# Kernel tuning notes

Measured on AMD Instinct MI355X. Metric: run time of the kernel, lower is better.

Reference implementation:

```python
import jax, jax.numpy as jnp
import numpy as np

D_MODEL = 1024
NUM_HEADS = 16
D_K = D_MODEL // NUM_HEADS
EPS = 1e-8  # torch F.cosine_similarity eps


def setup_inputs() -> dict:
    key = jax.random.key(0)
    ks = jax.random.split(key, 12)
    B, S = 2, 2048
    s = 1.0 / np.sqrt(D_MODEL)
    inp = {
        'q': jax.random.normal(ks[0], (B, S, D_MODEL), jnp.float32),
        'k': jax.random.normal(ks[1], (B, S, D_MODEL), jnp.float32),
        'v': jax.random.normal(ks[2], (B, S, D_MODEL), jnp.float32),
        'mask': jnp.ones((1, 1, 1, S), jnp.int32),
        'Wq': jax.random.normal(ks[3], (D_MODEL, D_MODEL), jnp.float32) * s,
        'bq': jax.random.normal(ks[4], (D_MODEL,), jnp.float32) * s,
        'Wk': jax.random.normal(ks[5], (D_MODEL, D_MODEL), jnp.float32) * s,
        'bk': jax.random.normal(ks[6], (D_MODEL,), jnp.float32) * s,
        'Wv': jax.random.normal(ks[7], (D_MODEL, D_MODEL), jnp.float32) * s,
        'bv': jax.random.normal(ks[8], (D_MODEL,), jnp.float32) * s,
        'Wo': jax.random.normal(ks[9], (D_MODEL, D_MODEL), jnp.float32) * s,
        'bo': jax.random.normal(ks[10], (D_MODEL,), jnp.float32) * s,
    }
    return inp


def _cosine(a, b):
    # torch F.cosine_similarity along last dim with eps clamp on each norm
    na = jnp.maximum(jnp.linalg.norm(a, axis=-1), EPS)
    nb = jnp.maximum(jnp.linalg.norm(b, axis=-1), EPS)
    return jnp.sum(a * b, axis=-1) / (na * nb)


def reference(q, k, v, mask, Wq, bq, Wk, bk, Wv, bv, Wo, bo):
    B, S, _ = q.shape
    H, dk = NUM_HEADS, D_K
    # projections -> [B, H, S, dk]
    def proj(x, W, b):
        return (x @ W.T + b).reshape(B, S, H, dk).transpose(0, 2, 1, 3)
    Q = proj(q, Wq, bq)
    K = proj(k, Wk, bk)
    V = proj(v, Wv, bv)
    scores = jnp.einsum('bhqd,bhkd->bhqk', Q, K) / np.sqrt(dk)
    # per-(batch, head) cosine-similarity bias between mean query and mean value
    cos = _cosine(Q.mean(axis=2), V.mean(axis=2))  # [B, H]
    bias = cos[:, :, None, None]
    scores = scores + bias * 0.5 + bias * 0.3  # empathy + equilibrium biases
    scores = jnp.where(mask == 0, -1e9, scores)
    probs = jax.nn.softmax(scores, axis=-1)
    attn = jnp.einsum('bhqk,bhkd->bhqd', probs, V)
    attn = attn.transpose(0, 2, 1, 3).reshape(B, S, H * dk)
    out = attn @ Wo.T + bo
    return out, jnp.mean(bias)
```

## Files before the change

### kernel.cpp

```cpp
#include <hip/hip_runtime.h>
#include <math.h>

#define SB 2
#define SS 2048
#define SD 1024
#define SH 16
#define SDK 64
#define MROWS (SB*SS)

#define L2E 1.44269504088896341f
#define SCL2E (0.125f * L2E)
#define M0 8.0f

typedef float  f32x4  __attribute__((ext_vector_type(4)));
typedef float  f32x16 __attribute__((ext_vector_type(16)));
typedef __bf16 bf16x8 __attribute__((ext_vector_type(8)));
typedef short  short8 __attribute__((ext_vector_type(8), may_alias));
typedef short  short4a __attribute__((ext_vector_type(4), may_alias));
typedef float  floatx4a __attribute__((ext_vector_type(4), may_alias));
typedef unsigned uint4v __attribute__((ext_vector_type(4)));

__device__ __forceinline__ short f2bf(float f) {
    unsigned u = __float_as_uint(f);
    u += 0x7fffu + ((u >> 16) & 1u);
    return (short)(u >> 16);
}
__device__ __forceinline__ float bf2f(short v) {
    return __uint_as_float(((unsigned)(unsigned short)v) << 16);
}
__device__ __forceinline__ bf16x8 ldb(const short* p) {
    short8 v = *(const short8*)p;
    return __builtin_bit_cast(bf16x8, v);
}
__device__ __forceinline__ unsigned cvtpk(float lo, float hi) {
    unsigned r;
    asm("v_cvt_pk_bf16_f32 %0, %1, %2" : "=v"(r) : "v"(lo), "v"(hi));
    return r;
}
__device__ __forceinline__ void gload16(const short* g, short* l) {
    __builtin_amdgcn_global_load_lds(
        (const __attribute__((address_space(1))) unsigned*)g,
        (__attribute__((address_space(3))) unsigned*)l, 16, 0, 0);
}
#define MFMA(a, b, c)   __builtin_amdgcn_mfma_f32_16x16x32_bf16((a), (b), (c), 0, 0, 0)
#define MFMA32(a, b, c) __builtin_amdgcn_mfma_f32_32x32x16_bf16((a), (b), (c), 0, 0, 0)

__global__ __launch_bounds__(256) void conv_all(
    const float* __restrict__ q, const float* __restrict__ k, const float* __restrict__ v,
    const float* __restrict__ Wq, const float* __restrict__ Wk,
    const float* __restrict__ Wv, const float* __restrict__ Wo,
    short* __restrict__ qb, short* __restrict__ kb, short* __restrict__ vb,
    short* __restrict__ wqb, short* __restrict__ wkb,
    short* __restrict__ wvb, short* __restrict__ wob)
{
    const int y = blockIdx.y;
    const float* src; short* dst; int n;
    switch (y) {
        case 0: src = q;  dst = qb;  n = MROWS * SD; break;
        case 1: src = k;  dst = kb;  n = MROWS * SD; break;
        case 2: src = v;  dst = vb;  n = MROWS * SD; break;
        case 3: src = Wq; dst = wqb; n = SD * SD; break;
        case 4: src = Wk; dst = wkb; n = SD * SD; break;
        case 5: src = Wv; dst = wvb; n = SD * SD; break;
        default: src = Wo; dst = wob; n = SD * SD; break;
    }
    int i = (blockIdx.x * 256 + threadIdx.x) * 4;
    if (i >= n) return;
    floatx4a x = *(const floatx4a*)(src + i);
    short4a o;
    o[0] = f2bf(x[0]); o[1] = f2bf(x[1]); o[2] = f2bf(x[2]); o[3] = f2bf(x[3]);
    *(short4a*)(dst + i) = o;
}

__global__ __launch_bounds__(256) void gemm128(
    const short* __restrict__ X0, const short* __restrict__ X1, const short* __restrict__ X2,
    const short* __restrict__ W0, const short* __restrict__ W1, const short* __restrict__ W2,
    const float* __restrict__ bias0, const float* __restrict__ bias1, const float* __restrict__ bias2,
    short* __restrict__ O0, short* __restrict__ O1, short* __restrict__ O2)
{
    const int z = blockIdx.z;
    const short* X = (z == 0) ? X0 : (z == 1) ? X1 : X2;
    const short* W = (z == 0) ? W0 : (z == 1) ? W1 : W2;
    const float* Bv = (z == 0) ? bias0 : (z == 1) ? bias1 : bias2;
    short* Obf = (z == 0) ? O0 : (z == 1) ? O1 : O2;

    const int bm = 4 * blockIdx.x + (blockIdx.y >> 3);
    const int bn = blockIdx.y & 7;
    const int tid = threadIdx.x;
    const int w = tid >> 6, lane = tid & 63, g = lane >> 4, r = lane & 15;
    const int wm = w >> 1, wn = w & 1;

    __shared__ short As[128 * 32];
    __shared__ short Bsm[128 * 32];

    const int srow = tid >> 2, sseg = tid & 3;
    const short* ga0 = X + (size_t)(bm * 128 + srow) * SD + sseg * 8;
    const short* ga1 = X + (size_t)(bm * 128 + 64 + srow) * SD + sseg * 8;
    const short* gb0 = W + (size_t)(bn * 128 + srow) * SD + sseg * 8;
    const short* gb1 = W + (size_t)(bn * 128 + 64 + srow) * SD + sseg * 8;
    short* la0 = As + tid * 8;
    short* la1 = As + 2048 + tid * 8;
    short* lb0 = Bsm + tid * 8;
    short* lb1 = Bsm + 2048 + tid * 8;

    f32x4 acc[4][4];
    const f32x4 zz = {0.f, 0.f, 0.f, 0.f};
#pragma unroll
    for (int i = 0; i < 4; i++)
#pragma unroll
        for (int j = 0; j < 4; j++) acc[i][j] = zz;

    for (int kt = 0; kt < 32; ++kt) {
        if (kt) __syncthreads();
        gload16(ga0 + kt * 32, la0);
        gload16(ga1 + kt * 32, la1);
        gload16(gb0 + kt * 32, lb0);
        gload16(gb1 + kt * 32, lb1);
        __syncthreads();
        bf16x8 af[4], bfr[4];
#pragma unroll
        for (int mf = 0; mf < 4; mf++) af[mf] = ldb(&As[(wm * 64 + mf * 16 + r) * 32 + g * 8]);
#pragma unroll
        for (int nf = 0; nf < 4; nf++) bfr[nf] = ldb(&Bsm[(wn * 64 + nf * 16 + r) * 32 + g * 8]);
#pragma unroll
        for (int mf = 0; mf < 4; mf++)
#pragma unroll
            for (int nf = 0; nf < 4; nf++)
                acc[mf][nf] = MFMA(af[mf], bfr[nf], acc[mf][nf]);
    }

    float bv[4];
#pragma unroll
    for (int nf = 0; nf < 4; nf++) bv[nf] = Bv[bn * 128 + wn * 64 + nf * 16 + r];

#pragma unroll
    for (int mf = 0; mf < 4; mf++)
#pragma unroll
        for (int nf = 0; nf < 4; nf++)
#pragma unroll
            for (int rr = 0; rr < 4; rr++) {
                int row = bm * 128 + wm * 64 + mf * 16 + g * 4 + rr;
                int col = bn * 128 + wn * 64 + nf * 16 + r;
                float v = acc[mf][nf][rr] + bv[nf];
                int b = row >> 11, s = row & 2047, h = col >> 6, d = col & 63;
                Obf[(((size_t)(b * SH + h)) * SS + s) * SDK + d] = f2bf(v);
            }
}

__global__ __launch_bounds__(256) void gemm_out(
    const short* __restrict__ X, const short* __restrict__ W,
    const float* __restrict__ Bv, float* __restrict__ OutF)
{
    const int i = blockIdx.x;
    const int xcd = i & 7, j = i >> 3;
    const int bm = 4 * xcd + (j & 3);
    const int bn = j >> 2;
    const int tid = threadIdx.x;
    const int w = tid >> 6, lane = tid & 63, g = lane >> 4, r = lane & 15;
    const int wm = w >> 1, wn = w & 1;

    __shared__ short As[128 * 32];
    __shared__ short Bsm[64 * 32];

    const int srow = tid >> 2, sseg = tid & 3;
    const short* ga0 = X + (size_t)(bm * 128 + srow) * SD + sseg * 8;
    const short* ga1 = X + (size_t)(bm * 128 + 64 + srow) * SD + sseg * 8;
    const short* gb0 = W + (size_t)(bn * 64 + srow) * SD + sseg * 8;
    short* la0 = As + tid * 8;
    short* la1 = As + 2048 + tid * 8;
    short* lb0 = Bsm + tid * 8;

    f32x4 acc[4][2];
    const f32x4 zz = {0.f, 0.f, 0.f, 0.f};
#pragma unroll
    for (int a = 0; a < 4; a++) { acc[a][0] = zz; acc[a][1] = zz; }

    for (int kt = 0; kt < 32; ++kt) {
        if (kt) __syncthreads();
        gload16(ga0 + kt * 32, la0);
        gload16(ga1 + kt * 32, la1);
        gload16(gb0 + kt * 32, lb0);
        __syncthreads();
        bf16x8 af[4], bfr[2];
#pragma unroll
        for (int mf = 0; mf < 4; mf++) af[mf] = ldb(&As[(wm * 64 + mf * 16 + r) * 32 + g * 8]);
#pragma unroll
        for (int nf = 0; nf < 2; nf++) bfr[nf] = ldb(&Bsm[(wn * 32 + nf * 16 + r) * 32 + g * 8]);
#pragma unroll
        for (int mf = 0; mf < 4; mf++)
#pragma unroll
            for (int nf = 0; nf < 2; nf++)
                acc[mf][nf] = MFMA(af[mf], bfr[nf], acc[mf][nf]);
    }

    float bv[2];
#pragma unroll
    for (int nf = 0; nf < 2; nf++) bv[nf] = Bv[bn * 64 + wn * 32 + nf * 16 + r];

#pragma unroll
    for (int mf = 0; mf < 4; mf++)
#pragma unroll
        for (int nf = 0; nf < 2; nf++)
#pragma unroll
            for (int rr = 0; rr < 4; rr++) {
                int row = bm * 128 + wm * 64 + mf * 16 + g * 4 + rr;
                int col = bn * 64 + wn * 32 + nf * 16 + r;
                OutF[(size_t)row * SD + col] = acc[mf][nf][rr] + bv[nf];
            }
}

__global__ __launch_bounds__(256) void transpose_v(const short* __restrict__ Vh,
                                                   short* __restrict__ VhT)
{
    const int bh = blockIdx.x >> 5, st = blockIdx.x & 31;
    __shared__ short T[64][72];
    const int tid = threadIdx.x;
    const int r = tid >> 2, cseg = tid & 3;
    const short* src = Vh + ((size_t)bh * SS + st * 64 + r) * SDK + cseg * 16;
    *(short8*)&T[r][cseg * 16]     = ((const short8*)src)[0];
    *(short8*)&T[r][cseg * 16 + 8] = ((const short8*)src)[1];
    __syncthreads();
    short8 o0, o1;
#pragma unroll
    for (int j = 0; j < 8; j++) {
        o0[j] = T[cseg * 16 + j][r];
        o1[j] = T[cseg * 16 + 8 + j][r];
    }
    short* dst = VhT + ((size_t)bh * SDK + r) * SS + st * 64 + cseg * 16;
    ((short8*)dst)[0] = o0;
    ((short8*)dst)[1] = o1;
}

__global__ __launch_bounds__(256) void make_mb2(const int* __restrict__ mask,
                                                float* __restrict__ mb2)
{
    int i = blockIdx.x * 256 + threadIdx.x;
    if (i < SS) mb2[i] = ((mask[i] != 0) ? 0.f : -1.0e9f * L2E) - M0 * L2E;
}

__global__ __launch_bounds__(256, 4) void attn_v6(
    const short* __restrict__ Qh, const short* __restrict__ Kh,
    const short* __restrict__ VhT, const float* __restrict__ mb2,
    short* __restrict__ attnb)
{
    const int blk = blockIdx.x;
    const int xcd = blk & 7, j = blk >> 3;
    const int qc = j & 31, bh = xcd + 8 * (j >> 5);
    const int tid = threadIdx.x;
    const int w = tid >> 6, l = tid & 63;
    const int q5 = l & 31, h = l >> 5;
    const int qch = w & 1, kh = w >> 1;
    const int swk = q5 & 7;
    const int swv = (q5 ^ (q5 >> 2)) & 3;
    const int qbase = qc * 64 + qch * 32;
    const int kbase = kh * 1024;

    const short* Qg = Qh + ((size_t)bh * SS + qbase) * SDK;
    const short* Kg = Kh + (size_t)bh * SS * SDK;
    const short* Vt = VhT + (size_t)bh * SDK * SS;

    __shared__ short smem[16384];
    short* base = smem;

    bf16x8 qf[4];
#pragma unroll
    for (int t = 0; t < 4; t++)
        qf[t] = ldb(Qg + (size_t)q5 * SDK + t * 16 + h * 8);

    f32x16 oacc0, oacc1;
#pragma unroll
    for (int i = 0; i < 16; i++) { oacc0[i] = 0.f; oacc1[i] = 0.f; }
    float lsum = 0.f;

    const int ptid = tid & 127;
    short8 stK[2], stV[2];

#define STAGE_LOAD(TK)                                                          \
    {                                                                           \
        _Pragma("unroll")                                                       \
        for (int i_ = 0; i_ < 2; i_++) {                                        \
            int c_ = ptid + i_ * 128;                                           \
            int kr_ = c_ >> 3, ks_ = c_ & 7;                                    \
            stK[i_] = *(const short8*)(Kg + (size_t)(kbase + (TK) * 32 + kr_) * SDK + ks_ * 8); \
            int vr_ = c_ >> 2, vs_ = c_ & 3;                                    \
            stV[i_] = *(const short8*)(Vt + (size_t)vr_ * SS + kbase + (TK) * 32 + vs_ * 8);    \
        }                                                                       \
    }
#define STAGE_WRITE(BUF)                                                        \
    {                                                                           \
        short* kp_ = base + ((kh * 2 + (BUF)) * 2 + 0) * 2048;                  \
        short* vp_ = base + ((kh * 2 + (BUF)) * 2 + 1) * 2048;                  \
        _Pragma("unroll")                                                       \
        for (int i_ = 0; i_ < 2; i_++) {                                        \
            int c_ = ptid + i_ * 128;                                           \
            int kr_ = c_ >> 3, ks_ = c_ & 7;                                    \
            *(short8*)&kp_[(kr_ * 8 + (ks_ ^ (kr_ & 7))) * 8] = stK[i_];        \
            int vr_ = c_ >> 2, vs_ = c_ & 3;                                    \
            *(short8*)&vp_[(vr_ * 4 + (vs_ ^ ((vr_ ^ (vr_ >> 2)) & 3))) * 8] = stV[i_]; \
        }                                                                       \
    }
#define LDK(BUF, T) ldb(&base[((kh * 2 + (BUF)) * 2 + 0) * 2048 + (q5 * 8 + (((T) * 2 + h) ^ swk)) * 8])
#define LDV(BUF, G2, T) ldb(&base[((kh * 2 + (BUF)) * 2 + 1) * 2048 + ((q5 + 32 * (G2)) * 4 + (((T) * 2 + h) ^ swv)) * 8])

    STAGE_LOAD(0);
    STAGE_WRITE(0);
    __syncthreads();
    int cur = 0;

    for (int kt = 0; kt < 32; ++kt) {
        if (kt < 31) STAGE_LOAD(kt + 1);

        f32x16 sg0;
#pragma unroll
        for (int i = 0; i < 16; i++) sg0[i] = 0.f;
        __builtin_amdgcn_s_setprio(1);
#pragma unroll
        for (int t = 0; t < 4; t++) {
            bf16x8 kf = LDK(cur, t);
            sg0 = MFMA32(kf, qf[t], sg0);
        }
        __builtin_amdgcn_s_setprio(0);

        const float* mb_ = mb2 + kbase + kt * 32;
#pragma unroll
        for (int a = 0; a < 4; a++) {
            floatx4a m4 = *(const floatx4a*)(mb_ + a * 8 + 4 * h);
#pragma unroll
            for (int b3 = 0; b3 < 4; b3++) {
                float p0 = __builtin_amdgcn_exp2f(fmaf(sg0[a * 4 + b3], SCL2E, m4[b3]));
                sg0[a * 4 + b3] = p0;
                lsum += p0;
            }
        }

        __builtin_amdgcn_s_setprio(1);
#pragma unroll
        for (int t = 0; t < 2; t++) {
            const int b8 = t * 8;
            unsigned u0 = cvtpk(sg0[b8 + 0], sg0[b8 + 1]);
            unsigned u1 = cvtpk(sg0[b8 + 2], sg0[b8 + 3]);
            unsigned u2 = cvtpk(sg0[b8 + 4], sg0[b8 + 5]);
            unsigned u3 = cvtpk(sg0[b8 + 6], sg0[b8 + 7]);
            asm("v_permlane32_swap_b32 %0, %1" : "+v"(u0), "+v"(u2));
            asm("v_permlane32_swap_b32 %0, %1" : "+v"(u1), "+v"(u3));
            uint4v uw = {u0, u1, u2, u3};
            bf16x8 pa = __builtin_bit_cast(bf16x8, uw);
            bf16x8 vf0 = LDV(cur, 0, t);
            bf16x8 vf1 = LDV(cur, 1, t);
            oacc0 = MFMA32(pa, vf0, oacc0);
            oacc1 = MFMA32(pa, vf1, oacc1);
        }
        __builtin_amdgcn_s_setprio(0);

        if (kt < 31) STAGE_WRITE(cur ^ 1);
        __syncthreads();
        cur ^= 1;
    }
#undef STAGE_LOAD
#undef STAGE_WRITE
#undef LDK
#undef LDV

    __syncthreads();
    float* cm = (float*)smem;
    if (kh == 1) {
        float* dst = cm + (qch * 64 + l) * 33;
#pragma unroll
        for (int i = 0; i < 16; i++) { dst[i] = oacc0[i]; dst[16 + i] = oacc1[i]; }
        dst[32] = lsum;
    }
    __syncthreads();
    if (kh == 0) {
        const float* src = cm + (qch * 64 + l) * 33;
#pragma unroll
        for (int i = 0; i < 16; i++) { oacc0[i] += src[i]; oacc1[i] += src[16 + i]; }
        lsum += src[32];
        lsum += __shfl_xor(lsum, 32);
        float inv = 1.f / lsum;
        const int b = bh >> 4, hh = bh & 15;
#pragma unroll
        for (int i = 0; i < 16; i++) {
            int qrow = (i & 3) + 8 * (i >> 2) + 4 * h;
            float invq = __shfl(inv, (l & 32) + qrow);
            int qg = qbase + qrow;
            size_t ob = ((size_t)(b * SS + qg)) * SD + hh * SDK;
            attnb[ob + q5]      = f2bf(oacc0[i] * invq);
            attnb[ob + 32 + q5] = f2bf(oacc1[i] * invq);
        }
    }
}

__global__ __launch_bounds__(256) void bias_part(const short* __restrict__ Qh,
                                                 const short* __restrict__ VhT,
                                                 float* __restrict__ qpart,
                                                 float* __restrict__ vpart)
{
    const int bh = blockIdx.x >> 3, ch = blockIdx.x & 7;
    const int t = threadIdx.x;
    const int d = t & 63, c = t >> 6;
    const short* Qp = Qh + ((size_t)bh * SS + ch * 256 + c * 64) * SDK + d;
    float sq = 0.f;
    for (int s = 0; s < 64; s++) sq += bf2f(Qp[(size_t)s * SDK]);
    const short* Vp = VhT + ((size_t)bh * SDK + (t >> 2)) * SS + ch * 256 + (t & 3) * 64;
    float sv = 0.f;
    for (int s8 = 0; s8 < 8; s8++) {
        short8 v8 = *(const short8*)(Vp + s8 * 8);
#pragma unroll
        for (int jj = 0; jj < 8; jj++) sv += bf2f(v8[jj]);
    }
    __shared__ float SQ[4][64], SV[64][4];
    SQ[c][d] = sq; SV[t >> 2][t & 3] = sv;
    __syncthreads();
    if (t < 64) {
        qpart[((size_t)bh * 8 + ch) * 64 + t] = SQ[0][t] + SQ[1][t] + SQ[2][t] + SQ[3][t];
        vpart[((size_t)bh * 8 + ch) * 64 + t] = SV[t][0] + SV[t][1] + SV[t][2] + SV[t][3];
    }
}

__global__ __launch_bounds__(64) void bias_fin(const float* __restrict__ qpart,
                                               const float* __restrict__ vpart,
                                               float* __restrict__ biasbuf)
{
    const int bh = blockIdx.x;
    const int t = threadIdx.x;
    float qm = 0.f, vm = 0.f;
#pragma unroll
    for (int ch = 0; ch < 8; ch++) {
        qm += qpart[((size_t)bh * 8 + ch) * 64 + t];
        vm += vpart[((size_t)bh * 8 + ch) * 64 + t];
    }
    qm *= (1.f / 2048.f); vm *= (1.f / 2048.f);
    float dot = qm * vm, nq = qm * qm, nv = vm * vm;
#pragma unroll
    for (int m2 = 1; m2 < 64; m2 <<= 1) {
        dot += __shfl_xor(dot, m2);
        nq += __shfl_xor(nq, m2);
        nv += __shfl_xor(nv, m2);
    }
    if (t == 0) {
        float na = fmaxf(sqrtf(nq), 1e-8f);
        float nb = fmaxf(sqrtf(nv), 1e-8f);
        biasbuf[bh] = dot / (na * nb);
    }
}

__global__ __launch_bounds__(64) void bias_mean(const float* __restrict__ biasbuf,
                                                float* __restrict__ out, int idx)
{
    int t = threadIdx.x;
    float v = (t < 32) ? biasbuf[t] : 0.f;
#pragma unroll
    for (int m2 = 1; m2 < 32; m2 <<= 1) v += __shfl_xor(v, m2);
    if (t == 0) out[idx] = v * (1.f / 32.f);
}

extern "C" void kernel_launch(void* const* d_in, const int* in_sizes, int n_in,
                              void* d_out, int out_size, void* d_ws, size_t ws_size,
                              hipStream_t stream)
{
    const float* q  = (const float*)d_in[0];
    const float* k  = (const float*)d_in[1];
    const float* v  = (const float*)d_in[2];
    const int* mask = (const int*)d_in[3];
    const float* Wq = (const float*)d_in[4];
    const float* bq = (const float*)d_in[5];
    const float* Wk = (const float*)d_in[6];
    const float* bk = (const float*)d_in[7];
    const float* Wv = (const float*)d_in[8];
    const float* bv = (const float*)d_in[9];
    const float* Wo = (const float*)d_in[10];
    const float* bo = (const float*)d_in[11];
    float* out = (float*)d_out;

    const size_t QKV_B = (size_t)MROWS * SD * sizeof(short);
    const size_t W_B   = (size_t)SD * SD * sizeof(short);
    size_t off = 0;
    char* ws = (char*)d_ws;
    auto take = [&](size_t b) { void* p = ws + off; off += (b + 255) & ~(size_t)255; return p; };

    short* qb  = (short*)take(QKV_B);
    short* kb  = (short*)take(QKV_B);
    short* vb  = (short*)take(QKV_B);
    short* wqb = (short*)take(W_B);
    short* wkb = (short*)take(W_B);
    short* wvb = (short*)take(W_B);
    short* wob = (short*)take(W_B);
    short* Qh  = (short*)take(QKV_B);
    short* Kh  = (short*)take(QKV_B);
    short* Vh  = (short*)take(QKV_B);
    float* qpart = (float*)take(32 * 8 * 64 * sizeof(float));
    float* vpart = (float*)take(32 * 8 * 64 * sizeof(float));
    float* biasbuf = (float*)take(256);
    short* attnb = qb;
    short* VhT   = vb;
    float* mb2   = (float*)kb;

    conv_all<<<dim3(4096, 7), 256, 0, stream>>>(q, k, v, Wq, Wk, Wv, Wo,
                                                qb, kb, vb, wqb, wkb, wvb, wob);

    gemm128<<<dim3(SD / 128, MROWS / 128, 3), 256, 0, stream>>>(
        qb, kb, vb, wqb, wkb, wvb, bq, bk, bv, Qh, Kh, Vh);

    transpose_v<<<32 * 32, 256, 0, stream>>>(Vh, VhT);
    make_mb2<<<SS / 256, 256, 0, stream>>>(mask, mb2);

    bias_part<<<32 * 8, 256, 0, stream>>>(Qh, VhT, qpart, vpart);
    bias_fin<<<SB * SH, 64, 0, stream>>>(qpart, vpart, biasbuf);

    attn_v6<<<SB * SH * (SS / 64), 256, 0, stream>>>(Qh, Kh, VhT, mb2, attnb);

    gemm_out<<<512, 256, 0, stream>>>(attnb, wob, bo, out);

    bias_mean<<<1, 64, 0, stream>>>(biasbuf, out, out_size - 1);
}
```

Measured before the change: 147.8 us.

## Load K fragments directly from global into registers, bypassing LDS staging

K tiles are now loaded straight from global memory into per-lane MFMA operand registers with a register double buffer (ka/kb_), and only V goes through LDS. The loop is unrolled by two so the buffers alternate at compile time. This halves LDS footprint and removes the K LDS write/read traffic. In exchange it adds VGPR pressure and makes uncoalesced-ish per-lane global loads sit on the critical path. The combine epilogue is also reworked to fit the smaller shared buffer.

```diff
diff --git a/kernel.cpp b/kernel.cpp
--- a/kernel.cpp
+++ b/kernel.cpp
@@ -238,7 +238,7 @@
     if (i < SS) mb2[i] = ((mask[i] != 0) ? 0.f : -1.0e9f * L2E) - M0 * L2E;
 }
 
-__global__ __launch_bounds__(256, 4) void attn_v6(
+__global__ __launch_bounds__(256, 4) void attn_v7(
     const short* __restrict__ Qh, const short* __restrict__ Kh,
     const short* __restrict__ VhT, const float* __restrict__ mb2,
     short* __restrict__ attnb)
@@ -250,16 +250,15 @@
     const int w = tid >> 6, l = tid & 63;
     const int q5 = l & 31, h = l >> 5;
     const int qch = w & 1, kh = w >> 1;
-    const int swk = q5 & 7;
     const int swv = (q5 ^ (q5 >> 2)) & 3;
     const int qbase = qc * 64 + qch * 32;
     const int kbase = kh * 1024;
 
     const short* Qg = Qh + ((size_t)bh * SS + qbase) * SDK;
-    const short* Kg = Kh + (size_t)bh * SS * SDK;
+    const short* Kg = Kh + ((size_t)bh * SS + kbase) * SDK;
     const short* Vt = VhT + (size_t)bh * SDK * SS;
 
-    __shared__ short smem[16384];
+    __shared__ short smem[8192];
     short* base = smem;
 
     bf16x8 qf[4];
@@ -273,108 +272,115 @@
     float lsum = 0.f;
 
     const int ptid = tid & 127;
-    short8 stK[2], stV[2];
-
+    short8 stV[2];
+    bf16x8 ka[4], kb_[4];
+
+#define KLOAD(DST, TK)                                                          \
+    {                                                                           \
+        const short* Ktp_ = Kg + (size_t)((TK) * 32 + q5) * SDK;                \
+        _Pragma("unroll")                                                       \
+        for (int t = 0; t < 4; t++) DST[t] = ldb(Ktp_ + t * 16 + h * 8);        \
+    }
 #define STAGE_LOAD(TK)                                                          \
     {                                                                           \
         _Pragma("unroll")                                                       \
         for (int i_ = 0; i_ < 2; i_++) {                                        \
             int c_ = ptid + i_ * 128;                                           \
-            int kr_ = c_ >> 3, ks_ = c_ & 7;                                    \
-            stK[i_] = *(const short8*)(Kg + (size_t)(kbase + (TK) * 32 + kr_) * SDK + ks_ * 8); \
             int vr_ = c_ >> 2, vs_ = c_ & 3;                                    \
-            stV[i_] = *(const short8*)(Vt + (size_t)vr_ * SS + kbase + (TK) * 32 + vs_ * 8);    \
+            stV[i_] = *(const short8*)(Vt + (size_t)vr_ * SS + kbase + (TK) * 32 + vs_ * 8); \
         }                                                                       \
     }
 #define STAGE_WRITE(BUF)                                                        \
     {                                                                           \
-        short* kp_ = base + ((kh * 2 + (BUF)) * 2 + 0) * 2048;                  \
-        short* vp_ = base + ((kh * 2 + (BUF)) * 2 + 1) * 2048;                  \
+        short* vp_ = base + (kh * 2 + (BUF)) * 2048;                            \
         _Pragma("unroll")                                                       \
         for (int i_ = 0; i_ < 2; i_++) {                                        \
             int c_ = ptid + i_ * 128;                                           \
-            int kr_ = c_ >> 3, ks_ = c_ & 7;                                    \
-            *(short8*)&kp_[(kr_ * 8 + (ks_ ^ (kr_ & 7))) * 8] = stK[i_];        \
             int vr_ = c_ >> 2, vs_ = c_ & 3;                                    \
             *(short8*)&vp_[(vr_ * 4 + (vs_ ^ ((vr_ ^ (vr_ >> 2)) & 3))) * 8] = stV[i_]; \
         }                                                                       \
     }
-#define LDK(BUF, T) ldb(&base[((kh * 2 + (BUF)) * 2 + 0) * 2048 + (q5 * 8 + (((T) * 2 + h) ^ swk)) * 8])
-#define LDV(BUF, G2, T) ldb(&base[((kh * 2 + (BUF)) * 2 + 1) * 2048 + ((q5 + 32 * (G2)) * 4 + (((T) * 2 + h) ^ swv)) * 8])
-
+#define LDV(BUF, G2, T) ldb(&base[(kh * 2 + (BUF)) * 2048 + ((q5 + 32 * (G2)) * 4 + (((T) * 2 + h) ^ swv)) * 8])
+
+#define STEP(CK, NK, KT, CUR)                                                   \
+    {                                                                           \
+        if ((KT) < 31) { KLOAD(NK, (KT) + 1); STAGE_LOAD((KT) + 1); }           \
+        f32x16 sg0;                                                             \
+        _Pragma("unroll")                                                       \
+        for (int i = 0; i < 16; i++) sg0[i] = 0.f;                              \
+        __builtin_amdgcn_s_setprio(1);                                          \
+        _Pragma("unroll")                                                       \
+        for (int t = 0; t < 4; t++) sg0 = MFMA32(CK[t], qf[t], sg0);            \
+        __builtin_amdgcn_s_setprio(0);                                          \
+        const float* mb_ = mb2 + kbase + (KT) * 32;                             \
+        _Pragma("unroll")                                                       \
+        for (int a = 0; a < 4; a++) {                                           \
+            floatx4a m4 = *(const floatx4a*)(mb_ + a * 8 + 4 * h);              \
+            _Pragma("unroll")                                                   \
+            for (int b3 = 0; b3 < 4; b3++) {                                    \
+                float p0 = __builtin_amdgcn_exp2f(fmaf(sg0[a * 4 + b3], SCL2E, m4[b3])); \
+                sg0[a * 4 + b3] = p0;                                           \
+                lsum += p0;                                                     \
+            }                                                                   \
+        }                                                                       \
+        __builtin_amdgcn_s_setprio(1);                                          \
+        _Pragma("unroll")                                                       \
+        for (int t = 0; t < 2; t++) {                                           \
+            const int b8 = t * 8;                                               \
+            unsigned u0 = cvtpk(sg0[b8 + 0], sg0[b8 + 1]);                      \
+            unsigned u1 = cvtpk(sg0[b8 + 2], sg0[b8 + 3]);                      \
+            unsigned u2 = cvtpk(sg0[b8 + 4], sg0[b8 + 5]);                      \
+            unsigned u3 = cvtpk(sg0[b8 + 6], sg0[b8 + 7]);                      \
+            asm("v_permlane32_swap_b32 %0, %1" : "+v"(u0), "+v"(u2));           \
+            asm("v_permlane32_swap_b32 %0, %1" : "+v"(u1), "+v"(u3));           \
+            uint4v uw = {u0, u1, u2, u3};                                       \
+            bf16x8 pa = __builtin_bit_cast(bf16x8, uw);                         \
+            bf16x8 vf0 = LDV(CUR, 0, t);                                        \
+            bf16x8 vf1 = LDV(CUR, 1, t);                                        \
+            oacc0 = MFMA32(pa, vf0, oacc0);                                     \
+            oacc1 = MFMA32(pa, vf1, oacc1);                                     \
+        }                                                                       \
+        __builtin_amdgcn_s_setprio(0);                                          \
+        if ((KT) < 31) STAGE_WRITE((CUR) ^ 1);                                  \
+        __syncthreads();                                                        \
+    }
+
+    KLOAD(ka, 0);
     STAGE_LOAD(0);
     STAGE_WRITE(0);
     __syncthreads();
-    int cur = 0;
-
-    for (int kt = 0; kt < 32; ++kt) {
-        if (kt < 31) STAGE_LOAD(kt + 1);
-
-        f32x16 sg0;
-#pragma unroll
-        for (int i = 0; i < 16; i++) sg0[i] = 0.f;
-        __builtin_amdgcn_s_setprio(1);
-#pragma unroll
-        for (int t = 0; t < 4; t++) {
-            bf16x8 kf = LDK(cur, t);
-            sg0 = MFMA32(kf, qf[t], sg0);
-        }
-        __builtin_amdgcn_s_setprio(0);
-
-        const float* mb_ = mb2 + kbase + kt * 32;
-#pragma unroll
-        for (int a = 0; a < 4; a++) {
-            floatx4a m4 = *(const floatx4a*)(mb_ + a * 8 + 4 * h);
-#pragma unroll
-            for (int b3 = 0; b3 < 4; b3++) {
-                float p0 = __builtin_amdgcn_exp2f(fmaf(sg0[a * 4 + b3], SCL2E, m4[b3]));
-                sg0[a * 4 + b3] = p0;
-                lsum += p0;
-            }
-        }
-
-        __builtin_amdgcn_s_setprio(1);
-#pragma unroll
-        for (int t = 0; t < 2; t++) {
-            const int b8 = t * 8;
-            unsigned u0 = cvtpk(sg0[b8 + 0], sg0[b8 + 1]);
-            unsigned u1 = cvtpk(sg0[b8 + 2], sg0[b8 + 3]);
-            unsigned u2 = cvtpk(sg0[b8 + 4], sg0[b8 + 5]);
-            unsigned u3 = cvtpk(sg0[b8 + 6], sg0[b8 + 7]);
-            asm("v_permlane32_swap_b32 %0, %1" : "+v"(u0), "+v"(u2));
-            asm("v_permlane32_swap_b32 %0, %1" : "+v"(u1), "+v"(u3));
-            uint4v uw = {u0, u1, u2, u3};
-            bf16x8 pa = __builtin_bit_cast(bf16x8, uw);
-            bf16x8 vf0 = LDV(cur, 0, t);
-            bf16x8 vf1 = LDV(cur, 1, t);
-            oacc0 = MFMA32(pa, vf0, oacc0);
-            oacc1 = MFMA32(pa, vf1, oacc1);
-        }
-        __builtin_amdgcn_s_setprio(0);
-
-        if (kt < 31) STAGE_WRITE(cur ^ 1);
-        __syncthreads();
-        cur ^= 1;
-    }
+
+    for (int kt = 0; kt < 32; kt += 2) {
+        STEP(ka, kb_, kt, 0);
+        STEP(kb_, ka, kt + 1, 1);
+    }
+#undef KLOAD
 #undef STAGE_LOAD
 #undef STAGE_WRITE
-#undef LDK
 #undef LDV
+#undef STEP
 
     __syncthreads();
     float* cm = (float*)smem;
     if (kh == 1) {
-        float* dst = cm + (qch * 64 + l) * 33;
+        float* dst = cm + (qch * 64 + l) * 32;
 #pragma unroll
         for (int i = 0; i < 16; i++) { dst[i] = oacc0[i]; dst[16 + i] = oacc1[i]; }
-        dst[32] = lsum;
     }
     __syncthreads();
     if (kh == 0) {
-        const float* src = cm + (qch * 64 + l) * 33;
+        const float* src = cm + (qch * 64 + l) * 32;
 #pragma unroll
         for (int i = 0; i < 16; i++) { oacc0[i] += src[i]; oacc1[i] += src[16 + i]; }
-        lsum += src[32];
+    }
+    __syncthreads();
+    {
+        float* ls = cm;
+        ls[(kh * 2 + qch) * 64 + l] = lsum;
+    }
+    __syncthreads();
+    if (kh == 0) {
+        lsum += cm[(2 + qch) * 64 + l];
         lsum += __shfl_xor(lsum, 32);
         float inv = 1.f / lsum;
         const int b = bh >> 4, hh = bh & 15;
@@ -507,7 +513,7 @@
     bias_part<<<32 * 8, 256, 0, stream>>>(Qh, VhT, qpart, vpart);
     bias_fin<<<SB * SH, 64, 0, stream>>>(qpart, vpart, biasbuf);
 
-    attn_v6<<<SB * SH * (SS / 64), 256, 0, stream>>>(Qh, Kh, VhT, mb2, attnb);
+    attn_v7<<<SB * SH * (SS / 64), 256, 0, stream>>>(Qh, Kh, VhT, mb2, attnb);
 
     gemm_out<<<512, 256, 0, stream>>>(attnb, wob, bo, out);
 
```

Result: slower. 218.1 us (+47.6%).

## Compute V projection transposed directly, dropping separate V transpose kernel

Applied to the files above, without the earlier changes.

The V projection is split out of the batched QKV GEMM into a new gemm_vt kernel that computes Wv·Xᵀ, so each output row is a head dimension and is written straight into the transposed [B,H,dk,S] layout the attention kernel reads. This removes the transpose_v kernel launch and its full read-and-write pass over V. In exchange, V gets its own launch of 512 64x128-tile blocks instead of sharing the 3-way batched GEMM, and its epilogue does scalar strided stores plus a per-element bias load. VhT now has its own buffer instead of reusing vb.

```diff
diff --git a/kernel.cpp b/kernel.cpp
--- a/kernel.cpp
+++ b/kernel.cpp
@@ -73,16 +73,16 @@
 }
 
 __global__ __launch_bounds__(256) void gemm128(
-    const short* __restrict__ X0, const short* __restrict__ X1, const short* __restrict__ X2,
-    const short* __restrict__ W0, const short* __restrict__ W1, const short* __restrict__ W2,
-    const float* __restrict__ bias0, const float* __restrict__ bias1, const float* __restrict__ bias2,
-    short* __restrict__ O0, short* __restrict__ O1, short* __restrict__ O2)
+    const short* __restrict__ X0, const short* __restrict__ X1,
+    const short* __restrict__ W0, const short* __restrict__ W1,
+    const float* __restrict__ bias0, const float* __restrict__ bias1,
+    short* __restrict__ O0, short* __restrict__ O1)
 {
     const int z = blockIdx.z;
-    const short* X = (z == 0) ? X0 : (z == 1) ? X1 : X2;
-    const short* W = (z == 0) ? W0 : (z == 1) ? W1 : W2;
-    const float* Bv = (z == 0) ? bias0 : (z == 1) ? bias1 : bias2;
-    short* Obf = (z == 0) ? O0 : (z == 1) ? O1 : O2;
+    const short* X = (z == 0) ? X0 : X1;
+    const short* W = (z == 0) ? W0 : W1;
+    const float* Bv = (z == 0) ? bias0 : bias1;
+    short* Obf = (z == 0) ? O0 : O1;
 
     const int bm = 4 * blockIdx.x + (blockIdx.y >> 3);
     const int bn = blockIdx.y & 7;
@@ -147,6 +147,68 @@
             }
 }
 
+__global__ __launch_bounds__(256) void gemm_vt(
+    const short* __restrict__ Wv, const short* __restrict__ Xv,
+    const float* __restrict__ Bv, short* __restrict__ VhT)
+{
+    const int i = blockIdx.x;
+    const int xcd = i & 7, j = i >> 3;
+    const int bm = j >> 2;
+    const int bn = 4 * xcd + (j & 3);
+    const int tid = threadIdx.x;
+    const int w = tid >> 6, lane = tid & 63, g = lane >> 4, r = lane & 15;
+    const int wm = w >> 1, wn = w & 1;
+
+    __shared__ short As[64 * 32];
+    __shared__ short Bsm[128 * 32];
+
+    const int srow = tid >> 2, sseg = tid & 3;
+    const short* ga0 = Wv + (size_t)(bm * 64 + srow) * SD + sseg * 8;
+    const short* gb0 = Xv + (size_t)(bn * 128 + srow) * SD + sseg * 8;
+    const short* gb1 = Xv + (size_t)(bn * 128 + 64 + srow) * SD + sseg * 8;
+    short* la0 = As + tid * 8;
+    short* lb0 = Bsm + tid * 8;
+    short* lb1 = Bsm + 2048 + tid * 8;
+
+    f32x4 acc[2][4];
+    const f32x4 zz = {0.f, 0.f, 0.f, 0.f};
+#pragma unroll
+    for (int a = 0; a < 2; a++)
+#pragma unroll
+        for (int b2 = 0; b2 < 4; b2++) acc[a][b2] = zz;
+
+    for (int kt = 0; kt < 32; ++kt) {
+        if (kt) __syncthreads();
+        gload16(ga0 + kt * 32, la0);
+        gload16(gb0 + kt * 32, lb0);
+        gload16(gb1 + kt * 32, lb1);
+        __syncthreads();
+        bf16x8 af[2], bfr[4];
+#pragma unroll
+        for (int mf = 0; mf < 2; mf++) af[mf] = ldb(&As[(wm * 32 + mf * 16 + r) * 32 + g * 8]);
+#pragma unroll
+        for (int nf = 0; nf < 4; nf++) bfr[nf] = ldb(&Bsm[(wn * 64 + nf * 16 + r) * 32 + g * 8]);
+#pragma unroll
+        for (int mf = 0; mf < 2; mf++)
+#pragma unroll
+            for (int nf = 0; nf < 4; nf++)
+                acc[mf][nf] = MFMA(af[mf], bfr[nf], acc[mf][nf]);
+    }
+
+#pragma unroll
+    for (int mf = 0; mf < 2; mf++)
+#pragma unroll
+        for (int nf = 0; nf < 4; nf++)
+#pragma unroll
+            for (int rr = 0; rr < 4; rr++) {
+                int row = bm * 64 + wm * 32 + mf * 16 + g * 4 + rr;
+                int col = bn * 128 + wn * 64 + nf * 16 + r;
+                int h = row >> 6, d = row & 63, b = col >> 11, s = col & 2047;
+                VhT[(((size_t)(b * SH + h)) * SDK + d) * SS + s] =
+                    f2bf(acc[mf][nf][rr] + Bv[row]);
+            }
+}
+
 __global__ __launch_bounds__(256) void gemm_out(
     const short* __restrict__ X, const short* __restrict__ W,
     const float* __restrict__ Bv, float* __restrict__ OutF)
@@ -207,28 +269,6 @@
                 int col = bn * 64 + wn * 32 + nf * 16 + r;
                 OutF[(size_t)row * SD + col] = acc[mf][nf][rr] + bv[nf];
             }
-}
-
-__global__ __launch_bounds__(256) void transpose_v(const short* __restrict__ Vh,
-                                                   short* __restrict__ VhT)
-{
-    const int bh = blockIdx.x >> 5, st = blockIdx.x & 31;
-    __shared__ short T[64][72];
-    const int tid = threadIdx.x;
-    const int r = tid >> 2, cseg = tid & 3;
-    const short* src = Vh + ((size_t)bh * SS + st * 64 + r) * SDK + cseg * 16;
-    *(short8*)&T[r][cseg * 16]     = ((const short8*)src)[0];
-    *(short8*)&T[r][cseg * 16 + 8] = ((const short8*)src)[1];
-    __syncthreads();
-    short8 o0, o1;
-#pragma unroll
-    for (int j = 0; j < 8; j++) {
-        o0[j] = T[cseg * 16 + j][r];
-        o1[j] = T[cseg * 16 + 8 + j][r];
-    }
-    short* dst = VhT + ((size_t)bh * SDK + r) * SS + st * 64 + cseg * 16;
-    ((short8*)dst)[0] = o0;
-    ((short8*)dst)[1] = o1;
 }
 
 __global__ __launch_bounds__(256) void make_mb2(const int* __restrict__ mask,
@@ -487,21 +527,21 @@
     short* wob = (short*)take(W_B);
     short* Qh  = (short*)take(QKV_B);
     short* Kh  = (short*)take(QKV_B);
-    short* Vh  = (short*)take(QKV_B);
+    short* VhT = (short*)take(QKV_B);
     float* qpart = (float*)take(32 * 8 * 64 * sizeof(float));
     float* vpart = (float*)take(32 * 8 * 64 * sizeof(float));
     float* biasbuf = (float*)take(256);
     short* attnb = qb;
-    short* VhT   = vb;
     float* mb2   = (float*)kb;
 
     conv_all<<<dim3(4096, 7), 256, 0, stream>>>(q, k, v, Wq, Wk, Wv, Wo,
                                                 qb, kb, vb, wqb, wkb, wvb, wob);
 
-    gemm128<<<dim3(SD / 128, MROWS / 128, 3), 256, 0, stream>>>(
-        qb, kb, vb, wqb, wkb, wvb, bq, bk, bv, Qh, Kh, Vh);
-
-    transpose_v<<<32 * 32, 256, 0, stream>>>(Vh, VhT);
+    gemm128<<<dim3(SD / 128, MROWS / 128, 2), 256, 0, stream>>>(
+        qb, kb, wqb, wkb, bq, bk, Qh, Kh);
+
+    gemm_vt<<<512, 256, 0, stream>>>(wvb, vb, bv, VhT);
+
     make_mb2<<<SS / 256, 256, 0, stream>>>(mask, mb2);
 
     bias_part<<<32 * 8, 256, 0, stream>>>(Qh, VhT, qpart, vpart);
```

After: 152.7 us. +3.3%, slower.

## Widen attention blocks to 128 queries with 512 threads sharing K/V tiles

Applied to the files above, without the earlier changes.

The attention kernel now runs 512 threads per block, covering 128 query rows instead of 64. Four query wave-pairs share each staged K/V tile in LDS, which halves global K/V traffic per query, and each thread stages one vector instead of two. The final cross-half reduction is reorganised so the row sums travel through a separate LDS pass, which adds extra barriers. The grid is half as large, and launch bounds of 512×4 may squeeze registers and risk spills.

```diff
diff --git a/kernel.cpp b/kernel.cpp
--- a/kernel.cpp
+++ b/kernel.cpp
@@ -238,21 +238,21 @@
     if (i < SS) mb2[i] = ((mask[i] != 0) ? 0.f : -1.0e9f * L2E) - M0 * L2E;
 }
 
-__global__ __launch_bounds__(256, 4) void attn_v6(
+__global__ __launch_bounds__(512, 4) void attn_v8(
     const short* __restrict__ Qh, const short* __restrict__ Kh,
     const short* __restrict__ VhT, const float* __restrict__ mb2,
     short* __restrict__ attnb)
 {
     const int blk = blockIdx.x;
     const int xcd = blk & 7, j = blk >> 3;
-    const int qc = j & 31, bh = xcd + 8 * (j >> 5);
+    const int qc = j & 15, bh = xcd + 8 * (j >> 4);
     const int tid = threadIdx.x;
     const int w = tid >> 6, l = tid & 63;
     const int q5 = l & 31, h = l >> 5;
-    const int qch = w & 1, kh = w >> 1;
+    const int qch = w & 3, kh = w >> 2;
     const int swk = q5 & 7;
     const int swv = (q5 ^ (q5 >> 2)) & 3;
-    const int qbase = qc * 64 + qch * 32;
+    const int qbase = qc * 128 + qch * 32;
     const int kbase = kh * 1024;
 
     const short* Qg = Qh + ((size_t)bh * SS + qbase) * SDK;
@@ -272,32 +272,24 @@
     for (int i = 0; i < 16; i++) { oacc0[i] = 0.f; oacc1[i] = 0.f; }
     float lsum = 0.f;
 
-    const int ptid = tid & 127;
-    short8 stK[2], stV[2];
+    const int ptid = tid & 255;
+    short8 stK, stV;
 
 #define STAGE_LOAD(TK)                                                          \
     {                                                                           \
-        _Pragma("unroll")                                                       \
-        for (int i_ = 0; i_ < 2; i_++) {                                        \
-            int c_ = ptid + i_ * 128;                                           \
-            int kr_ = c_ >> 3, ks_ = c_ & 7;                                    \
-            stK[i_] = *(const short8*)(Kg + (size_t)(kbase + (TK) * 32 + kr_) * SDK + ks_ * 8); \
-            int vr_ = c_ >> 2, vs_ = c_ & 3;                                    \
-            stV[i_] = *(const short8*)(Vt + (size_t)vr_ * SS + kbase + (TK) * 32 + vs_ * 8);    \
-        }                                                                       \
+        int kr_ = ptid >> 3, ks_ = ptid & 7;                                    \
+        stK = *(const short8*)(Kg + (size_t)(kbase + (TK) * 32 + kr_) * SDK + ks_ * 8); \
+        int vr_ = ptid >> 2, vs_ = ptid & 3;                                    \
+        stV = *(const short8*)(Vt + (size_t)vr_ * SS + kbase + (TK) * 32 + vs_ * 8);    \
     }
 #define STAGE_WRITE(BUF)                                                        \
     {                                                                           \
         short* kp_ = base + ((kh * 2 + (BUF)) * 2 + 0) * 2048;                  \
         short* vp_ = base + ((kh * 2 + (BUF)) * 2 + 1) * 2048;                  \
-        _Pragma("unroll")                                                       \
-        for (int i_ = 0; i_ < 2; i_++) {                                        \
-            int c_ = ptid + i_ * 128;                                           \
-            int kr_ = c_ >> 3, ks_ = c_ & 7;                                    \
-            *(short8*)&kp_[(kr_ * 8 + (ks_ ^ (kr_ & 7))) * 8] = stK[i_];        \
-            int vr_ = c_ >> 2, vs_ = c_ & 3;                                    \
-            *(short8*)&vp_[(vr_ * 4 + (vs_ ^ ((vr_ ^ (vr_ >> 2)) & 3))) * 8] = stV[i_]; \
-        }                                                                       \
+        int kr_ = ptid >> 3, ks_ = ptid & 7;                                    \
+        *(short8*)&kp_[(kr_ * 8 + (ks_ ^ (kr_ & 7))) * 8] = stK;                \
+        int vr_ = ptid >> 2, vs_ = ptid & 3;                                    \
+        *(short8*)&vp_[(vr_ * 4 + (vs_ ^ ((vr_ ^ (vr_ >> 2)) & 3))) * 8] = stV; \
     }
 #define LDK(BUF, T) ldb(&base[((kh * 2 + (BUF)) * 2 + 0) * 2048 + (q5 * 8 + (((T) * 2 + h) ^ swk)) * 8])
 #define LDV(BUF, G2, T) ldb(&base[((kh * 2 + (BUF)) * 2 + 1) * 2048 + ((q5 + 32 * (G2)) * 4 + (((T) * 2 + h) ^ swv)) * 8])
@@ -364,17 +356,24 @@
     __syncthreads();
     float* cm = (float*)smem;
     if (kh == 1) {
-        float* dst = cm + (qch * 64 + l) * 33;
+        float* dst = cm + (qch * 64 + l) * 32;
 #pragma unroll
         for (int i = 0; i < 16; i++) { dst[i] = oacc0[i]; dst[16 + i] = oacc1[i]; }
-        dst[32] = lsum;
     }
     __syncthreads();
     if (kh == 0) {
-        const float* src = cm + (qch * 64 + l) * 33;
+        const float* src = cm + (qch * 64 + l) * 32;
 #pragma unroll
         for (int i = 0; i < 16; i++) { oacc0[i] += src[i]; oacc1[i] += src[16 + i]; }
-        lsum += src[32];
+    }
+    __syncthreads();
+    {
+        float* ls = cm;
+        ls[(kh * 4 + qch) * 64 + l] = lsum;
+    }
+    __syncthreads();
+    if (kh == 0) {
+        lsum += cm[(4 + qch) * 64 + l];
         lsum += __shfl_xor(lsum, 32);
         float inv = 1.f / lsum;
         const int b = bh >> 4, hh = bh & 15;
@@ -507,7 +506,7 @@
     bias_part<<<32 * 8, 256, 0, stream>>>(Qh, VhT, qpart, vpart);
     bias_fin<<<SB * SH, 64, 0, stream>>>(qpart, vpart, biasbuf);
 
-    attn_v6<<<SB * SH * (SS / 64), 256, 0, stream>>>(Qh, Kh, VhT, mb2, attnb);
+    attn_v8<<<SB * SH * (SS / 128), 512, 0, stream>>>(Qh, Kh, VhT, mb2, attnb);
 
     gemm_out<<<512, 256, 0, stream>>>(attnb, wob, bo, out);
 
```

Result: faster. 141.2 us, median of 3 (-4.5%).
